# Optimization experiments

Hardware: AMD Instinct MI355X
Metric: run time of the kernel (lower is better)

Reference implementation:

```python
import jax, jax.numpy as jnp
import numpy as np

HEADS = 16
HEAD_DIM = 32
WINDOW = 64  # kernel_size = 2*WINDOW + 1 = 129
NEG = -1e30


def setup_inputs() -> dict:
    key = jax.random.key(0)
    ks = jax.random.split(key, 9)
    B, T, D, G = 4, 8192, HEADS * HEAD_DIM, 64
    x = jax.random.normal(ks[0], (B, T, D), jnp.float32)
    def W(k):
        return jax.random.normal(k, (D, D), jnp.float32) * 0.02
    def b(k):
        return jax.random.normal(k, (D,), jnp.float32) * 0.02
    return {
        "x": x,
        "Wq": W(ks[1]), "bq": b(ks[2]),
        "Wk": W(ks[3]), "bk": b(ks[4]),
        "Wv": W(ks[5]), "bv": b(ks[6]),
        "Wo": W(ks[7]), "bo": b(ks[8]),
        "global_idx": jnp.arange(G, dtype=jnp.int64 if jax.config.jax_enable_x64 else jnp.int32),
    }


def _sparse_global_attn(x, Wq, bq, Wk, bk, Wv, bv, Wo, bo, global_idx):
    B, T, D = x.shape
    H, d, w = HEADS, HEAD_DIM, WINDOW
    scale = 1.0 / (d ** 0.5)

    def proj(W, b):
        # (B,T,D) -> (B,H,T,d)
        return (x @ W + b).reshape(B, T, H, d).transpose(0, 2, 1, 3)

    q, k, v = proj(Wq, bq), proj(Wk, bk), proj(Wv, bv)

    offsets = jnp.arange(-w, w + 1)  # (K,)
    K = offsets.shape[0]

    # Local band scores: score[b,h,t,j] = <q[t], k[t+offset_j]>, computed
    # offset-by-offset via roll to avoid a (B,H,T,K,d) gather.
    def score_step(_, o):
        s = jnp.einsum('bhtd,bhtd->bht', q, jnp.roll(k, -o, axis=2))
        return None, s
    _, loc = jax.lax.scan(score_step, None, offsets)  # (K,B,H,T)
    loc = jnp.moveaxis(loc, 0, -1) * scale            # (B,H,T,K)

    pos = jnp.arange(T)[:, None] + offsets[None, :]   # (T,K)
    valid = (pos >= 0) & (pos < T)
    loc = jnp.where(valid[None, None], loc, NEG)

    # Global-token scores (global tokens shared across the batch)
    k_g = k[:, :, global_idx, :]                      # (B,H,G,d)
    v_g = v[:, :, global_idx, :]
    gsc = jnp.einsum('bhtd,bhgd->bhtg', q, k_g) * scale  # (B,H,T,G)

    # Joint softmax over [local window | global tokens] (duplicates where a
    # global token lies inside the local window, matching the original).
    attn = jax.nn.softmax(jnp.concatenate([loc, gsc], axis=-1), axis=-1)
    a_loc = jnp.moveaxis(attn[..., :K], -1, 0)        # (K,B,H,T)
    a_g = attn[..., K:]                               # (B,H,T,G)

    def ctx_step(acc, oa):
        o, a = oa
        return acc + a[..., None] * jnp.roll(v, -o, axis=2), None
    ctx, _ = jax.lax.scan(ctx_step, jnp.zeros_like(q), (offsets, a_loc))
    ctx = ctx + jnp.einsum('bhtg,bhgd->bhtd', a_g, v_g)  # (B,H,T,d)

    out = ctx.transpose(0, 2, 1, 3).reshape(B, T, D)
    return out @ Wo + bo


def reference(x, Wq, bq, Wk, bk, Wv, bv, Wo, bo, global_idx):
    return _sparse_global_attn(x, Wq, bq, Wk, bk, Wv, bv, Wo, bo, global_idx)
```

## Files before the change

### kernel.cpp

```cpp
#include <hip/hip_runtime.h>
#include <hip/hip_bf16.h>
#include <cstdint>
#include <cstddef>

using bf16 = __hip_bfloat16;
typedef __bf16 bf16x8 __attribute__((ext_vector_type(8)));
typedef __bf16 bf16x4 __attribute__((ext_vector_type(4)));
typedef float f32x4 __attribute__((ext_vector_type(4)));

constexpr int BB = 4;
constexpr int TS = 8192;
constexpr int NH = 16;
constexpr int HD = 32;
constexpr int DM = 512;
constexpr int NQKV = 1536;
constexpr int NG = 64;

#define MFMA16(a, b, c) __builtin_amdgcn_mfma_f32_16x16x32_bf16((a), (b), (c), 0, 0, 0)

__device__ __forceinline__ bf16x8 ld8(const bf16* p) { return *(const bf16x8*)p; }
__device__ __forceinline__ bf16x4 ld4(const bf16* p) { return *(const bf16x4*)p; }
__device__ __forceinline__ unsigned short b16bits(bf16 v) { return __builtin_bit_cast(unsigned short, v); }

__device__ __forceinline__ void gl_lds16(const bf16* g, void* l) {
  __builtin_amdgcn_global_load_lds((const __attribute__((address_space(1))) void*)g,
                                   (__attribute__((address_space(3))) void*)l, 16, 0, 0);
}

__global__ void prep_kernel(const float* __restrict__ x,
                            const float* __restrict__ Wq, const float* __restrict__ bq,
                            const float* __restrict__ Wk, const float* __restrict__ bk,
                            const float* __restrict__ Wv, const float* __restrict__ bv,
                            const float* __restrict__ Wo,
                            bf16* __restrict__ xb, bf16* __restrict__ Wt,
                            bf16* __restrict__ Wot, float* __restrict__ bqkv) {
  const int64_t stride = (int64_t)gridDim.x * blockDim.x;
  const int64_t i0 = (int64_t)blockIdx.x * blockDim.x + threadIdx.x;
  const float4* x4 = (const float4*)x;
  ushort4* xb4 = (ushort4*)xb;
  for (int64_t i = i0; i < (int64_t)BB * TS * DM / 4; i += stride) {
    float4 v = x4[i];
    ushort4 o;
    o.x = b16bits(__float2bfloat16(v.x));
    o.y = b16bits(__float2bfloat16(v.y));
    o.z = b16bits(__float2bfloat16(v.z));
    o.w = b16bits(__float2bfloat16(v.w));
    xb4[i] = o;
  }
  for (int64_t i = i0; i < (int64_t)NQKV * DM; i += stride) {
    const int n = (int)(i >> 9), k = (int)(i & 511);
    const float* W = (n < 512) ? Wq : ((n < 1024) ? Wk : Wv);
    Wt[i] = __float2bfloat16(W[(size_t)k * DM + (n & 511)]);
  }
  for (int64_t i = i0; i < (int64_t)DM * DM; i += stride) {
    const int n = (int)(i >> 9), k = (int)(i & 511);
    Wot[i] = __float2bfloat16(Wo[(size_t)k * DM + n]);
  }
  for (int64_t i = i0; i < NQKV; i += stride)
    bqkv[i] = (i < 512) ? bq[i] : ((i < 1024) ? bk[i - 512] : bv[i - 1024]);
}

template <bool F32OUT, bool WVT>
__global__ __launch_bounds__(512) void gemm_bias(const bf16* __restrict__ A,
                                                 const bf16* __restrict__ Bt,
                                                 const float* __restrict__ bias,
                                                 void* __restrict__ Cv,
                                                 bf16* __restrict__ vt,
                                                 int M, int N, int K, int cpx) {
  __shared__ __attribute__((aligned(16))) char smem[147456];
  const int tid = threadIdx.x;
  const int lane = tid & 63, wid = tid >> 6;
  const int grp = lane >> 4, col = lane & 15;
  const int bid = (blockIdx.x & 7) * cpx + (blockIdx.x >> 3);
  const int NT = N >> 7;
  const int mt = bid / NT, nt = bid % NT;
  const int m0 = mt << 8, n0 = nt << 7;
  const int wm = wid >> 1, wn = wid & 1;
  f32x4 acc[4][4] = {};
  const int KT = K >> 6;

  auto stage = [&](int kt) {
    char* buf = smem + (kt % 3) * 49152;
    #pragma unroll
    for (int c = 0; c < 4; ++c) {
      const int idx = c * 512 + tid;
      const int row = idx >> 3, sl = idx & 7;
      const int koff = ((sl ^ (row & 7)) << 3) + (kt << 6);
      gl_lds16(A + (size_t)(m0 + row) * K + koff, buf + idx * 16);
    }
    #pragma unroll
    for (int c = 0; c < 2; ++c) {
      const int idx = c * 512 + tid;
      const int row = idx >> 3, sl = idx & 7;
      const int koff = ((sl ^ (row & 7)) << 3) + (kt << 6);
      gl_lds16(Bt + (size_t)(n0 + row) * K + koff, buf + 32768 + idx * 16);
    }
  };

  stage(0);
  stage(1);
  for (int kt = 0; kt < KT; ++kt) {
    if (kt + 2 < KT) stage(kt + 2);
    __builtin_amdgcn_sched_barrier(0);
    if (kt + 2 < KT)      asm volatile("s_waitcnt vmcnt(12)" ::: "memory");
    else if (kt + 1 < KT) asm volatile("s_waitcnt vmcnt(6)" ::: "memory");
    else                  asm volatile("s_waitcnt vmcnt(0)" ::: "memory");
    __builtin_amdgcn_sched_barrier(0);
    __builtin_amdgcn_s_barrier();
    __builtin_amdgcn_sched_barrier(0);
    const char* sA = smem + (kt % 3) * 49152;
    const char* sB = sA + 32768;
    bf16x8 af[2][4], bfr[2][4];
    #pragma unroll
    for (int ks = 0; ks < 2; ++ks)
      #pragma unroll
      for (int f = 0; f < 4; ++f) {
        const int ra = wm * 64 + f * 16 + col;
        af[ks][f] = *(const bf16x8*)(sA + ra * 128 + (((ks * 4 + grp) ^ (ra & 7)) << 4));
        const int rb = wn * 64 + f * 16 + col;
        bfr[ks][f] = *(const bf16x8*)(sB + rb * 128 + (((ks * 4 + grp) ^ (rb & 7)) << 4));
      }
    #pragma unroll
    for (int ks = 0; ks < 2; ++ks) {
      __builtin_amdgcn_s_setprio(1);
      #pragma unroll
      for (int i = 0; i < 4; ++i)
        #pragma unroll
        for (int j = 0; j < 4; ++j)
          acc[i][j] = MFMA16(af[ks][i], bfr[ks][j], acc[i][j]);
      __builtin_amdgcn_s_setprio(0);
    }
    __builtin_amdgcn_sched_barrier(0);
    __builtin_amdgcn_s_barrier();
    __builtin_amdgcn_sched_barrier(0);
  }
  const bool wv = WVT && (n0 >= 1024);
  if (!wv) {
    #pragma unroll
    for (int i = 0; i < 4; ++i)
      #pragma unroll
      for (int j = 0; j < 4; ++j) {
        const int n = n0 + wn * 64 + j * 16 + col;
        const float bz = bias[n];
        #pragma unroll
        for (int r = 0; r < 4; ++r) {
          const int m = m0 + wm * 64 + i * 16 + grp * 4 + r;
          const float v = acc[i][j][r] + bz;
          if (F32OUT)
            ((float*)Cv)[(size_t)m * N + n] = v;
          else
            ((bf16*)Cv)[(size_t)m * N + n] = __float2bfloat16(v);
        }
      }
  } else {
    __syncthreads();
    bf16* lt = (bf16*)smem;
    #pragma unroll
    for (int i = 0; i < 4; ++i)
      #pragma unroll
      for (int j = 0; j < 4; ++j) {
        const int nl = wn * 64 + j * 16 + col;
        const float bz = bias[n0 + nl];
        #pragma unroll
        for (int r = 0; r < 4; ++r) {
          const int ml = wm * 64 + i * 16 + grp * 4 + r;
          lt[nl * 264 + (ml ^ ((nl & 7) << 4))] = __float2bfloat16(acc[i][j][r] + bz);
        }
      }
    __syncthreads();
    const int row = tid >> 2, q = tid & 3;
    const int b = m0 >> 13, t0 = m0 & 8191;
    bf16* dst = vt + (size_t)(b * DM + (n0 & 511) + row) * TS + t0 + q * 64;
    const bf16* srcl = lt + row * 264;
    #pragma unroll
    for (int c = 0; c < 8; ++c)
      *(bf16x8*)(dst + c * 8) =
          *(const bf16x8*)(srcl + ((q * 64 + c * 8) ^ ((row & 7) << 4)));
  }
}

__global__ void vgt_kernel(const bf16* __restrict__ vt, const int* __restrict__ gidx,
                           bf16* __restrict__ vtp, bf16* __restrict__ vgt) {
  const int64_t stride = (int64_t)gridDim.x * blockDim.x;
  const int64_t i0 = (int64_t)blockIdx.x * blockDim.x + threadIdx.x;
  for (int64_t i = i0; i < 512; i += stride) {
    if (i < 64) vtp[i - 64] = __float2bfloat16(0.f);
    else vtp[(size_t)2048 * TS + (i - 64)] = __float2bfloat16(0.f);
  }
  for (int64_t i = i0; i < (int64_t)2048 * NG; i += stride) {
    const int row = (int)(i >> 6), g = (int)(i & 63);
    const int gi = gidx[g];
    vgt[i] = vt[(size_t)row * TS + gi];
  }
}

__global__ __launch_bounds__(256) void attn_kernel(const bf16* __restrict__ qkv,
                                                   const bf16* __restrict__ vt,
                                                   const bf16* __restrict__ vgt,
                                                   const int* __restrict__ gidx,
                                                   bf16* __restrict__ ctx) {
  constexpr int VST = 216;
  constexpr int VGST = 88;
  __shared__ __attribute__((aligned(16))) char smem[35840];
  bf16* sV = (bf16*)smem;
  bf16* sVg = (bf16*)(smem + 13824);
  bf16* sK = (bf16*)(smem + 19456);
  bf16* sKg = (bf16*)(smem + 31744);

  const int tid = threadIdx.x, wid = tid >> 6, lane = tid & 63;
  const int grp = lane >> 4, col = lane & 15;
  const int bid = (blockIdx.x & 7) * 1024 + (blockIdx.x >> 3);
  const int tile = bid & 127, h = (bid >> 7) & 15, b = bid >> 11;
  const int t0b = tile * 64;
  const int kbb = t0b - 64;
  const int bh = b * NH + h;
  const bf16* base = qkv + (size_t)b * TS * NQKV;
  const bf16* kpl = base + 512 + h * 32;

  #pragma unroll
  for (int it = 0; it < 3; ++it) {
    const int idx = it * 256 + tid;
    const int row = idx >> 2, part = idx & 3;
    const int tok = min(max(kbb + row, 0), TS - 1);
    gl_lds16(kpl + (size_t)tok * NQKV + ((part ^ (row & 3)) << 3), sK + idx * 8);
  }
  {
    const int row = tid >> 2, part = tid & 3;
    const int gi = gidx[row];
    gl_lds16(kpl + (size_t)gi * NQKV + ((part ^ (row & 3)) << 3), sKg + tid * 8);
  }
  {
    const bf16* vr = vt + (size_t)(bh * HD + (tid >> 3)) * TS + kbb;
    #pragma unroll
    for (int i = 0; i < 4; ++i) {
      const int c = i * 8 + (tid & 7);
      if (c < 27) *(bf16x8*)(sV + (tid >> 3) * VST + c * 8) = ld8(vr + c * 8);
    }
  }
  {
    const int row = tid >> 3, c = tid & 7;
    *(bf16x8*)(sVg + row * VGST + c * 8) = ld8(vgt + (size_t)(bh * HD + row) * NG + c * 8);
  }
  __syncthreads();

  const int qt = t0b + wid * 16;
  const int offw = wid * 16;

  const bf16x8 qf = ld8(base + (size_t)(qt + col) * NQKV + h * 32 + grp * 8);
  const f32x4 z = {0.f, 0.f, 0.f, 0.f};
  f32x4 s[13];
  #pragma unroll
  for (int f = 0; f < 9; ++f) {
    const int row = offw + f * 16 + col;
    bf16x8 kf = ld8(sK + row * 32 + ((grp ^ (row & 3)) << 3));
    s[f] = MFMA16(kf, qf, z);
  }
  #pragma unroll
  for (int f = 0; f < 4; ++f) {
    const int row = f * 16 + col;
    bf16x8 kf = ld8(sKg + row * 32 + ((grp ^ (row & 3)) << 3));
    s[9 + f] = MFMA16(kf, qf, z);
  }
  const float scale = 0.17677669529663688f;
  float mx = -3e38f;
  const bool interior = (tile >= 1) & (tile <= 126);
  if (interior) {
    #pragma unroll
    for (int f = 0; f < 13; ++f) {
      #pragma unroll
      for (int r = 0; r < 4; ++r) {
        float v = s[f][r] * scale;
        if (f == 0) v = (grp * 4 + r >= col) ? v : -1e30f;
        if (f == 8) v = (grp * 4 + r <= col) ? v : -1e30f;
        s[f][r] = v;
        mx = fmaxf(mx, v);
      }
    }
  } else {
    #pragma unroll
    for (int f = 0; f < 13; ++f) {
      #pragma unroll
      for (int r = 0; r < 4; ++r) {
        float v = s[f][r] * scale;
        if (f < 9) {
          const int j = f * 16 + grp * 4 + r;
          const int pos = qt - 64 + j;
          const bool valid = (j >= col) & (j <= col + 128) & (pos >= 0) & (pos < TS);
          v = valid ? v : -1e30f;
        }
        s[f][r] = v;
        mx = fmaxf(mx, v);
      }
    }
  }
  mx = fmaxf(mx, __shfl_xor(mx, 16));
  mx = fmaxf(mx, __shfl_xor(mx, 32));
  float sum = 0.f;
  bf16x8 pb[7];
  #pragma unroll
  for (int f = 0; f < 13; ++f) {
    const int pr = (f < 9) ? (f >> 1) : (5 + ((f - 9) >> 1));
    const int hf = (f < 9) ? (f & 1) : ((f - 9) & 1);
    #pragma unroll
    for (int r = 0; r < 4; ++r) {
      float p = __expf(s[f][r] - mx);
      sum += p;
      pb[pr][hf * 4 + r] = (__bf16)__float2bfloat16(p);
    }
  }
  #pragma unroll
  for (int r = 0; r < 4; ++r) pb[4][4 + r] = (__bf16)__float2bfloat16(0.f);
  sum += __shfl_xor(sum, 16);
  sum += __shfl_xor(sum, 32);
  const float sm = 1.0f / sum;

  f32x4 c0 = z, c1 = z;
  const bf16* sVr0 = sV + col * VST;
  const bf16* sVr1 = sV + (col + 16) * VST;
  #pragma unroll
  for (int i = 0; i < 5; ++i) {
    const int kk = offw + i * 32 + grp * 4;
    bf16x8 a0 = __builtin_shufflevector(ld4(sVr0 + kk), ld4(sVr0 + kk + 16),
                                        0, 1, 2, 3, 4, 5, 6, 7);
    bf16x8 a1 = __builtin_shufflevector(ld4(sVr1 + kk), ld4(sVr1 + kk + 16),
                                        0, 1, 2, 3, 4, 5, 6, 7);
    c0 = MFMA16(a0, pb[i], c0);
    c1 = MFMA16(a1, pb[i], c1);
  }
  const bf16* sVg0 = sVg + col * VGST;
  const bf16* sVg1 = sVg + (col + 16) * VGST;
  #pragma unroll
  for (int i = 0; i < 2; ++i) {
    const int kk = i * 32 + grp * 4;
    bf16x8 a0 = __builtin_shufflevector(ld4(sVg0 + kk), ld4(sVg0 + kk + 16),
                                        0, 1, 2, 3, 4, 5, 6, 7);
    bf16x8 a1 = __builtin_shufflevector(ld4(sVg1 + kk), ld4(sVg1 + kk + 16),
                                        0, 1, 2, 3, 4, 5, 6, 7);
    c0 = MFMA16(a0, pb[5 + i], c0);
    c1 = MFMA16(a1, pb[5 + i], c1);
  }
  const int t = qt + col;
  bf16* op = ctx + ((size_t)(b * TS + t)) * DM + h * 32 + grp * 4;
  ushort4 o0, o1;
  o0.x = b16bits(__float2bfloat16(c0[0] * sm));
  o0.y = b16bits(__float2bfloat16(c0[1] * sm));
  o0.z = b16bits(__float2bfloat16(c0[2] * sm));
  o0.w = b16bits(__float2bfloat16(c0[3] * sm));
  o1.x = b16bits(__float2bfloat16(c1[0] * sm));
  o1.y = b16bits(__float2bfloat16(c1[1] * sm));
  o1.z = b16bits(__float2bfloat16(c1[2] * sm));
  o1.w = b16bits(__float2bfloat16(c1[3] * sm));
  *(ushort4*)op = o0;
  *(ushort4*)(op + 16) = o1;
}

extern "C" void kernel_launch(void* const* d_in, const int* in_sizes, int n_in,
                              void* d_out, int out_size, void* d_ws, size_t ws_size,
                              hipStream_t stream) {
  (void)in_sizes; (void)n_in; (void)out_size; (void)ws_size;
  const float* x = (const float*)d_in[0];
  const float* Wq = (const float*)d_in[1];
  const float* bq = (const float*)d_in[2];
  const float* Wk = (const float*)d_in[3];
  const float* bk = (const float*)d_in[4];
  const float* Wv = (const float*)d_in[5];
  const float* bv = (const float*)d_in[6];
  const float* Wo = (const float*)d_in[7];
  const float* bo = (const float*)d_in[8];
  const int* gidx = (const int*)d_in[9];
  float* out = (float*)d_out;

  char* ws = (char*)d_ws;
  size_t off = 0;
  auto alloc = [&](size_t bytes) -> void* {
    void* p = ws + off;
    off += (bytes + 255) & ~(size_t)255;
    return p;
  };
  bf16* xb = (bf16*)alloc((size_t)BB * TS * DM * 2);
  bf16* Wt = (bf16*)alloc((size_t)NQKV * DM * 2);
  bf16* Wot = (bf16*)alloc((size_t)DM * DM * 2);
  float* bqkv = (float*)alloc((size_t)NQKV * 4);
  bf16* qkv = (bf16*)alloc((size_t)BB * TS * NQKV * 2);
  bf16* vta = (bf16*)alloc(((size_t)2048 * TS + 512) * 2);
  bf16* vgt = (bf16*)alloc((size_t)2048 * NG * 2);
  bf16* ctx = xb;
  bf16* vt = vta + 64;

  prep_kernel<<<dim3(2048), dim3(256), 0, stream>>>(x, Wq, bq, Wk, bk, Wv, bv, Wo,
                                                    xb, Wt, Wot, bqkv);
  gemm_bias<false, true><<<dim3(1536), dim3(512), 0, stream>>>(xb, Wt, bqkv, qkv, vt,
                                                               BB * TS, NQKV, DM, 192);
  vgt_kernel<<<dim3(512), dim3(256), 0, stream>>>(vt, gidx, vt, vgt);
  attn_kernel<<<dim3(8192), dim3(256), 0, stream>>>(qkv, vt, vgt, gidx, ctx);
  gemm_bias<true, false><<<dim3(512), dim3(512), 0, stream>>>(ctx, Wot, bo, out, nullptr,
                                                              BB * TS, DM, DM, 64);
}
```

Baseline: 186.9 us.

## Enlarge GEMM tile to 256x256 with quadrant-interleaved prefetch pipeline

The bias GEMM moves from 256x128 tiles with a 3-stage buffer to 256x256 tiles split into four 128x128 quadrants, double-buffered in halves. Global-to-LDS loads for the next k-tiles are issued between quadrant compute phases, and the grid sizes are halved to match. The larger tile raises operand reuse per LDS load and cuts total global traffic. In exchange it roughly doubles accumulator registers, adds more barriers per k-step, and halves the number of blocks, which can hurt occupancy and wave balance across CUs.

```diff
diff --git a/kernel.cpp b/kernel.cpp
--- a/kernel.cpp
+++ b/kernel.cpp
@@ -61,121 +61,156 @@
 }
 
 template <bool F32OUT, bool WVT>
-__global__ __launch_bounds__(512) void gemm_bias(const bf16* __restrict__ A,
-                                                 const bf16* __restrict__ Bt,
-                                                 const float* __restrict__ bias,
-                                                 void* __restrict__ Cv,
-                                                 bf16* __restrict__ vt,
-                                                 int M, int N, int K, int cpx) {
-  __shared__ __attribute__((aligned(16))) char smem[147456];
+__global__ __launch_bounds__(512, 2) void gemm_bias(const bf16* __restrict__ A,
+                                                    const bf16* __restrict__ Bt,
+                                                    const float* __restrict__ bias,
+                                                    void* __restrict__ Cv,
+                                                    bf16* __restrict__ vt,
+                                                    int M, int N, int K, int cpx) {
+  __shared__ __attribute__((aligned(16))) char smem[131072];
   const int tid = threadIdx.x;
   const int lane = tid & 63, wid = tid >> 6;
   const int grp = lane >> 4, col = lane & 15;
   const int bid = (blockIdx.x & 7) * cpx + (blockIdx.x >> 3);
-  const int NT = N >> 7;
+  const int NT = N >> 8;
   const int mt = bid / NT, nt = bid % NT;
-  const int m0 = mt << 8, n0 = nt << 7;
-  const int wm = wid >> 1, wn = wid & 1;
-  f32x4 acc[4][4] = {};
+  const int m0 = mt << 8, n0 = nt << 8;
+  const int wm2 = wid >> 2, wn4 = wid & 3;
   const int KT = K >> 6;
-
-  auto stage = [&](int kt) {
-    char* buf = smem + (kt % 3) * 49152;
-    #pragma unroll
-    for (int c = 0; c < 4; ++c) {
-      const int idx = c * 512 + tid;
-      const int row = idx >> 3, sl = idx & 7;
-      const int koff = ((sl ^ (row & 7)) << 3) + (kt << 6);
-      gl_lds16(A + (size_t)(m0 + row) * K + koff, buf + idx * 16);
-    }
+  f32x4 acc[4][4][2] = {};
+
+  auto stageA = [&](int kt, int h) {
+    char* dst = smem + ((((kt & 1) << 1) + h) << 14);
     #pragma unroll
     for (int c = 0; c < 2; ++c) {
       const int idx = c * 512 + tid;
       const int row = idx >> 3, sl = idx & 7;
       const int koff = ((sl ^ (row & 7)) << 3) + (kt << 6);
-      gl_lds16(Bt + (size_t)(n0 + row) * K + koff, buf + 32768 + idx * 16);
+      gl_lds16(A + (size_t)(m0 + h * 128 + row) * K + koff, dst + idx * 16);
     }
   };
-
-  stage(0);
-  stage(1);
+  auto stageB = [&](int kt, int h) {
+    char* dst = smem + 65536 + ((((kt & 1) << 1) + h) << 14);
+    #pragma unroll
+    for (int c = 0; c < 2; ++c) {
+      const int idx = c * 512 + tid;
+      const int row = idx >> 3, sl = idx & 7;
+      const int koff = ((sl ^ (row & 7)) << 3) + (kt << 6);
+      gl_lds16(Bt + (size_t)(n0 + h * 128 + row) * K + koff, dst + idx * 16);
+    }
+  };
+
+  stageA(0, 0); stageB(0, 0); stageB(0, 1); stageA(0, 1);
+  stageA(1, 0); stageB(1, 0);
+  asm volatile("s_waitcnt vmcnt(4)" ::: "memory");
+  __builtin_amdgcn_sched_barrier(0);
+  __builtin_amdgcn_s_barrier();
+  __builtin_amdgcn_sched_barrier(0);
+
   for (int kt = 0; kt < KT; ++kt) {
-    if (kt + 2 < KT) stage(kt + 2);
-    __builtin_amdgcn_sched_barrier(0);
-    if (kt + 2 < KT)      asm volatile("s_waitcnt vmcnt(12)" ::: "memory");
-    else if (kt + 1 < KT) asm volatile("s_waitcnt vmcnt(6)" ::: "memory");
-    else                  asm volatile("s_waitcnt vmcnt(0)" ::: "memory");
-    __builtin_amdgcn_sched_barrier(0);
-    __builtin_amdgcn_s_barrier();
-    __builtin_amdgcn_sched_barrier(0);
-    const char* sA = smem + (kt % 3) * 49152;
-    const char* sB = sA + 32768;
-    bf16x8 af[2][4], bfr[2][4];
-    #pragma unroll
-    for (int ks = 0; ks < 2; ++ks)
+    const int d = kt & 1;
+    const char* sAb = smem + (d << 15);
+    const char* sBb = smem + 65536 + (d << 15);
+    #pragma unroll
+    for (int q = 0; q < 4; ++q) {
+      const char* sA = sAb + ((q >> 1) << 14);
+      const char* sB = sBb + ((q & 1) << 14);
+      bf16x8 af[4][2], bfr[2][2];
       #pragma unroll
       for (int f = 0; f < 4; ++f) {
-        const int ra = wm * 64 + f * 16 + col;
-        af[ks][f] = *(const bf16x8*)(sA + ra * 128 + (((ks * 4 + grp) ^ (ra & 7)) << 4));
-        const int rb = wn * 64 + f * 16 + col;
-        bfr[ks][f] = *(const bf16x8*)(sB + rb * 128 + (((ks * 4 + grp) ^ (rb & 7)) << 4));
-      }
-    #pragma unroll
-    for (int ks = 0; ks < 2; ++ks) {
+        const int ra = wm2 * 64 + f * 16 + col;
+        #pragma unroll
+        for (int ks = 0; ks < 2; ++ks)
+          af[f][ks] = *(const bf16x8*)(sA + ra * 128 + (((ks * 4 + grp) ^ (ra & 7)) << 4));
+      }
+      #pragma unroll
+      for (int j = 0; j < 2; ++j) {
+        const int rb = wn4 * 32 + j * 16 + col;
+        #pragma unroll
+        for (int ks = 0; ks < 2; ++ks)
+          bfr[j][ks] = *(const bf16x8*)(sB + rb * 128 + (((ks * 4 + grp) ^ (rb & 7)) << 4));
+      }
+      if (q == 0 && kt + 1 < KT) stageA(kt + 1, 1);
+      if (q == 1 && kt + 1 < KT) stageB(kt + 1, 1);
+      if (q == 2 && kt + 2 < KT) stageA(kt + 2, 0);
+      if (q == 3 && kt + 2 < KT) stageB(kt + 2, 0);
+      __builtin_amdgcn_sched_barrier(0);
+      __builtin_amdgcn_s_barrier();
+      __builtin_amdgcn_sched_barrier(0);
+      asm volatile("s_waitcnt lgkmcnt(0)" ::: "memory");
+      __builtin_amdgcn_sched_barrier(0);
       __builtin_amdgcn_s_setprio(1);
       #pragma unroll
-      for (int i = 0; i < 4; ++i)
+      for (int ks = 0; ks < 2; ++ks)
         #pragma unroll
-        for (int j = 0; j < 4; ++j)
-          acc[i][j] = MFMA16(af[ks][i], bfr[ks][j], acc[i][j]);
+        for (int f = 0; f < 4; ++f)
+          #pragma unroll
+          for (int j = 0; j < 2; ++j)
+            acc[q][f][j] = MFMA16(af[f][ks], bfr[j][ks], acc[q][f][j]);
       __builtin_amdgcn_s_setprio(0);
-    }
-    __builtin_amdgcn_sched_barrier(0);
-    __builtin_amdgcn_s_barrier();
-    __builtin_amdgcn_sched_barrier(0);
-  }
+      __builtin_amdgcn_sched_barrier(0);
+      if (q == 3) {
+        if (kt + 2 < KT) asm volatile("s_waitcnt vmcnt(4)" ::: "memory");
+        else             asm volatile("s_waitcnt vmcnt(0)" ::: "memory");
+        __builtin_amdgcn_sched_barrier(0);
+      }
+      __builtin_amdgcn_s_barrier();
+      __builtin_amdgcn_sched_barrier(0);
+    }
+  }
+
   const bool wv = WVT && (n0 >= 1024);
   if (!wv) {
     #pragma unroll
-    for (int i = 0; i < 4; ++i)
-      #pragma unroll
-      for (int j = 0; j < 4; ++j) {
-        const int n = n0 + wn * 64 + j * 16 + col;
+    for (int q = 0; q < 4; ++q)
+      #pragma unroll
+      for (int j = 0; j < 2; ++j) {
+        const int n = n0 + (q & 1) * 128 + wn4 * 32 + j * 16 + col;
         const float bz = bias[n];
         #pragma unroll
-        for (int r = 0; r < 4; ++r) {
-          const int m = m0 + wm * 64 + i * 16 + grp * 4 + r;
-          const float v = acc[i][j][r] + bz;
-          if (F32OUT)
-            ((float*)Cv)[(size_t)m * N + n] = v;
-          else
-            ((bf16*)Cv)[(size_t)m * N + n] = __float2bfloat16(v);
-        }
+        for (int f = 0; f < 4; ++f)
+          #pragma unroll
+          for (int r = 0; r < 4; ++r) {
+            const int m = m0 + (q >> 1) * 128 + wm2 * 64 + f * 16 + grp * 4 + r;
+            const float v = acc[q][f][j][r] + bz;
+            if (F32OUT)
+              ((float*)Cv)[(size_t)m * N + n] = v;
+            else
+              ((bf16*)Cv)[(size_t)m * N + n] = __float2bfloat16(v);
+          }
       }
   } else {
     __syncthreads();
     bf16* lt = (bf16*)smem;
     #pragma unroll
-    for (int i = 0; i < 4; ++i)
-      #pragma unroll
-      for (int j = 0; j < 4; ++j) {
-        const int nl = wn * 64 + j * 16 + col;
-        const float bz = bias[n0 + nl];
+    for (int p = 0; p < 2; ++p) {
+      if (p) __syncthreads();
+      #pragma unroll
+      for (int qm = 0; qm < 2; ++qm) {
+        const int q = qm * 2 + p;
         #pragma unroll
-        for (int r = 0; r < 4; ++r) {
-          const int ml = wm * 64 + i * 16 + grp * 4 + r;
-          lt[nl * 264 + (ml ^ ((nl & 7) << 4))] = __float2bfloat16(acc[i][j][r] + bz);
+        for (int j = 0; j < 2; ++j) {
+          const int nl = wn4 * 32 + j * 16 + col;
+          const float bz = bias[n0 + p * 128 + nl];
+          #pragma unroll
+          for (int f = 0; f < 4; ++f)
+            #pragma unroll
+            for (int r = 0; r < 4; ++r) {
+              const int ml = qm * 128 + wm2 * 64 + f * 16 + grp * 4 + r;
+              lt[nl * 264 + (ml ^ ((nl & 7) << 4))] = __float2bfloat16(acc[q][f][j][r] + bz);
+            }
         }
       }
-    __syncthreads();
-    const int row = tid >> 2, q = tid & 3;
-    const int b = m0 >> 13, t0 = m0 & 8191;
-    bf16* dst = vt + (size_t)(b * DM + (n0 & 511) + row) * TS + t0 + q * 64;
-    const bf16* srcl = lt + row * 264;
-    #pragma unroll
-    for (int c = 0; c < 8; ++c)
-      *(bf16x8*)(dst + c * 8) =
-          *(const bf16x8*)(srcl + ((q * 64 + c * 8) ^ ((row & 7) << 4)));
+      __syncthreads();
+      const int row = tid >> 2, qt4 = tid & 3;
+      const int b = m0 >> 13, t0 = m0 & 8191;
+      bf16* dst = vt + (size_t)(b * DM + (n0 & 511) + p * 128 + row) * TS + t0 + qt4 * 64;
+      const bf16* srcl = lt + row * 264;
+      #pragma unroll
+      for (int c = 0; c < 8; ++c)
+        *(bf16x8*)(dst + c * 8) =
+            *(const bf16x8*)(srcl + ((qt4 * 64 + c * 8) ^ ((row & 7) << 4)));
+    }
   }
 }
 
@@ -389,10 +424,10 @@
 
   prep_kernel<<<dim3(2048), dim3(256), 0, stream>>>(x, Wq, bq, Wk, bk, Wv, bv, Wo,
                                                     xb, Wt, Wot, bqkv);
-  gemm_bias<false, true><<<dim3(1536), dim3(512), 0, stream>>>(xb, Wt, bqkv, qkv, vt,
-                                                               BB * TS, NQKV, DM, 192);
+  gemm_bias<false, true><<<dim3(768), dim3(512), 0, stream>>>(xb, Wt, bqkv, qkv, vt,
+                                                              BB * TS, NQKV, DM, 96);
   vgt_kernel<<<dim3(512), dim3(256), 0, stream>>>(vt, gidx, vt, vgt);
   attn_kernel<<<dim3(8192), dim3(256), 0, stream>>>(qkv, vt, vgt, gidx, ctx);
-  gemm_bias<true, false><<<dim3(512), dim3(512), 0, stream>>>(ctx, Wot, bo, out, nullptr,
-                                                              BB * TS, DM, DM, 64);
-}
+  gemm_bias<true, false><<<dim3(256), dim3(512), 0, stream>>>(ctx, Wot, bo, out, nullptr,
+                                                              BB * TS, DM, DM, 32);
+}
```

New measurement: 187.0 us. Within noise of the previous version (+0.0%).
